# Kernel tuning notes

Measured on AMD Instinct MI355X. Metric: run time of the kernel, lower is better.

Reference implementation:

```python
import jax, jax.numpy as jnp
import numpy as np

N, E, D, H = 50000, 800000, 64, 4  # nodes, edges, dim_h, heads
NEG_SLOPE = 0.2
BN_EPS = 1e-5


def setup_inputs() -> dict:
    key = jax.random.key(0)
    ks = jax.random.split(key, 8)
    x = jax.random.normal(ks[0], (N, D), dtype=jnp.float32)
    edge_index = jax.random.randint(ks[1], (2, E), 0, N, dtype=jnp.int32)
    s = 1.0 / np.sqrt(D)
    W_lin = jax.random.normal(ks[2], (D, D), dtype=jnp.float32) * s
    b_lin = jnp.zeros((D,), dtype=jnp.float32)
    prelu_w = jnp.full((D,), 0.25, dtype=jnp.float32)
    W_gat = jax.random.normal(ks[3], (H * D, D), dtype=jnp.float32) * s  # maps D -> H*D
    att_src = jax.random.normal(ks[4], (H, D), dtype=jnp.float32) * 0.1
    att_dst = jax.random.normal(ks[5], (H, D), dtype=jnp.float32) * 0.1
    gat_bias = jnp.zeros((D,), dtype=jnp.float32)
    bn_gamma = jnp.ones((D,), dtype=jnp.float32)
    bn_beta = jnp.zeros((D,), dtype=jnp.float32)
    return dict(x=x, edge_index=edge_index, W_lin=W_lin, b_lin=b_lin,
                prelu_w=prelu_w, W_gat=W_gat, att_src=att_src, att_dst=att_dst,
                gat_bias=gat_bias, bn_gamma=bn_gamma, bn_beta=bn_beta)


def _gat_mod_fwd(x, edge_index, W_lin, b_lin, prelu_w, W_gat, att_src, att_dst,
                 gat_bias, bn_gamma, bn_beta):
    # --- pre linear + PReLU ---
    x = x @ W_lin.T + b_lin
    x = jnp.where(x >= 0, x, prelu_w * x)  # per-channel PReLU

    # --- GATConv (concat=False -> head mean), add_self_loops=True ---
    h = (x @ W_gat.T).reshape(N, H, D)              # [N,H,D]
    a_src = jnp.einsum('nhd,hd->nh', h, att_src)    # [N,H]
    a_dst = jnp.einsum('nhd,hd->nh', h, att_dst)    # [N,H]

    loop = jnp.arange(N, dtype=edge_index.dtype)
    src = jnp.concatenate([edge_index[0], loop])    # [E+N]
    dst = jnp.concatenate([edge_index[1], loop])

    e = jax.nn.leaky_relu(a_src[src] + a_dst[dst], NEG_SLOPE)   # [E+N, H]
    # segment softmax over destination nodes (self loops guarantee non-empty)
    emax = jax.ops.segment_max(e, dst, num_segments=N)          # [N,H]
    p = jnp.exp(e - emax[dst])
    denom = jax.ops.segment_sum(p, dst, num_segments=N)         # [N,H]
    alpha = p / denom[dst]                                      # [E+N,H]

    msg = h[src] * alpha[:, :, None]                            # [E+N,H,D]
    out = jax.ops.segment_sum(msg, dst, num_segments=N)         # [N,H,D]
    out = out.mean(axis=1) + gat_bias                           # [N,D]

    # --- BatchNorm1d (training: batch stats) + ReLU ---
    mean = out.mean(axis=0)
    var = out.var(axis=0)
    out = bn_gamma * (out - mean) * jax.lax.rsqrt(var + BN_EPS) + bn_beta
    return jax.nn.relu(out)


def reference(x, edge_index, W_lin, b_lin, prelu_w, W_gat, att_src, att_dst,
              gat_bias, bn_gamma, bn_beta):
    return _gat_mod_fwd(x, edge_index, W_lin, b_lin, prelu_w, W_gat, att_src,
                        att_dst, gat_bias, bn_gamma, bn_beta)
```

## Files before the change

kernel.cpp:

```cpp
#include <hip/hip_runtime.h>
#include <hip/hip_fp16.h>

#define NEG_SLOPE 0.2f
#define BN_EPS 1e-5f

constexpr int D = 64;
constexpr int H = 4;

constexpr int PSORT = 128;
constexpr int CHUNK_SHIFT = 13;
constexpr int CHUNK = 1 << CHUNK_SHIFT;
constexpr int MAXW2 = 12544;

typedef _Float16 half2_t __attribute__((ext_vector_type(2)));
typedef _Float16 half4_t __attribute__((ext_vector_type(4)));
typedef _Float16 half8_t __attribute__((ext_vector_type(8)));
typedef float f32x4_t __attribute__((ext_vector_type(4)));
typedef int i32x4 __attribute__((ext_vector_type(4)));

union Rec {
    i32x4 i4;
    struct { int idx; int pad; half4_t w; } f;
};

#define MFMA16(a, b, c) __builtin_amdgcn_mfma_f32_16x16x32_f16(a, b, c, 0, 0, 0)

#if __has_builtin(__builtin_amdgcn_fdot2)
#define FDOT2(a, b, c) __builtin_amdgcn_fdot2((a), (b), (c), false)
#else
#define FDOT2(a, b, c) ((c) + (float)(a)[0] * (float)(b)[0] + (float)(a)[1] * (float)(b)[1])
#endif

__device__ inline half2_t h2cast(unsigned int u) { return __builtin_bit_cast(half2_t, u); }

__device__ inline float lrelu(float v) { return (v >= 0.f) ? v : NEG_SLOPE * v; }

__device__ inline void split8(const float* p, bool ok, half8_t& hi, half8_t& lo) {
    float f[8];
    if (ok) {
        float4 a = *(const float4*)p;
        float4 b = *(const float4*)(p + 4);
        f[0] = a.x; f[1] = a.y; f[2] = a.z; f[3] = a.w;
        f[4] = b.x; f[5] = b.y; f[6] = b.z; f[7] = b.w;
    } else {
        #pragma unroll
        for (int j = 0; j < 8; j++) f[j] = 0.f;
    }
    #pragma unroll
    for (int j = 0; j < 8; j++) {
        _Float16 h = (_Float16)f[j];
        hi[j] = h;
        lo[j] = (_Float16)(f[j] - (float)h);
    }
}

__global__ __launch_bounds__(256) void k_node(
    const float* __restrict__ x,
    const float* __restrict__ W_lin, const float* __restrict__ b_lin,
    const float* __restrict__ prelu_w, const float* __restrict__ W_gat,
    const float* __restrict__ att_src, const float* __restrict__ att_dst,
    _Float16* __restrict__ hh, float* __restrict__ asrc_ws,
    float* __restrict__ adst_ws, int N)
{
    __shared__ _Float16 smem[32 * 264];
    _Float16* __restrict__ h_lds = smem;
    _Float16* __restrict__ x1hi  = smem;
    _Float16* __restrict__ x1lo  = smem + 32 * 72;

    const int t = threadIdx.x;
    const int w = t >> 6;
    const int l = t & 63;
    const int li = l & 15;
    const int lq = l >> 4;
    const int base = blockIdx.x * 32;
    const int nvalid = min(32, N - base);

    f32x4_t accA[2] = {};
    {
        half8_t blh[2], bll[2];
        const int n = 16 * w + li;
        #pragma unroll
        for (int ks = 0; ks < 2; ks++)
            split8(W_lin + n * 64 + 32 * ks + 8 * lq, true, blh[ks], bll[ks]);
        #pragma unroll
        for (int mt = 0; mt < 2; mt++) {
            const int row = base + 16 * mt + li;
            const bool ok = row < N;
            #pragma unroll
            for (int ks = 0; ks < 2; ks++) {
                half8_t ah, al;
                split8(x + (size_t)row * 64 + 32 * ks + 8 * lq, ok, ah, al);
                accA[mt] = MFMA16(ah, blh[ks], accA[mt]);
                accA[mt] = MFMA16(al, blh[ks], accA[mt]);
                accA[mt] = MFMA16(ah, bll[ks], accA[mt]);
            }
        }
    }

    {
        const int n = 16 * w + li;
        const float bl = b_lin[n];
        const float pw = prelu_w[n];
        #pragma unroll
        for (int mt = 0; mt < 2; mt++) {
            #pragma unroll
            for (int r = 0; r < 4; r++) {
                const int m = 16 * mt + lq * 4 + r;
                float v = accA[mt][r] + bl;
                v = (v >= 0.f) ? v : pw * v;
                _Float16 hi = (_Float16)v;
                x1hi[m * 72 + n] = hi;
                x1lo[m * 72 + n] = (_Float16)(v - (float)hi);
            }
        }
    }
    __syncthreads();

    half8_t xah[2][2], xal[2][2];
    #pragma unroll
    for (int mt = 0; mt < 2; mt++) {
        #pragma unroll
        for (int ks = 0; ks < 2; ks++) {
            const int off = (16 * mt + li) * 72 + 32 * ks + 8 * lq;
            xah[mt][ks] = *(const half8_t*)(&x1hi[off]);
            xal[mt][ks] = *(const half8_t*)(&x1lo[off]);
        }
    }
    f32x4_t accB[2][4] = {};
    #pragma unroll
    for (int nt = 0; nt < 4; nt++) {
        half8_t wh[2], wl[2];
        const int c = 64 * w + 16 * nt + li;
        #pragma unroll
        for (int ks = 0; ks < 2; ks++)
            split8(W_gat + (size_t)c * 64 + 32 * ks + 8 * lq, true, wh[ks], wl[ks]);
        #pragma unroll
        for (int mt = 0; mt < 2; mt++) {
            #pragma unroll
            for (int ks = 0; ks < 2; ks++) {
                accB[mt][nt] = MFMA16(xah[mt][ks], wh[ks], accB[mt][nt]);
                accB[mt][nt] = MFMA16(xal[mt][ks], wh[ks], accB[mt][nt]);
                accB[mt][nt] = MFMA16(xah[mt][ks], wl[ks], accB[mt][nt]);
            }
        }
    }

    {
        float asv[4], adv[4];
        #pragma unroll
        for (int nt = 0; nt < 4; nt++) {
            const int c = 64 * w + 16 * nt + li;
            asv[nt] = att_src[c];
            adv[nt] = att_dst[c];
        }
        #pragma unroll
        for (int mt = 0; mt < 2; mt++) {
            #pragma unroll
            for (int r = 0; r < 4; r++) {
                float s = 0.f, dsum = 0.f;
                #pragma unroll
                for (int nt = 0; nt < 4; nt++) {
                    s += accB[mt][nt][r] * asv[nt];
                    dsum += accB[mt][nt][r] * adv[nt];
                }
                #pragma unroll
                for (int off = 1; off < 16; off <<= 1) {
                    s += __shfl_xor(s, off, 64);
                    dsum += __shfl_xor(dsum, off, 64);
                }
                if (li == 0) {
                    const int m = 16 * mt + lq * 4 + r;
                    if (m < nvalid) {
                        asrc_ws[(size_t)(base + m) * H + w] = s;
                        adst_ws[(size_t)(base + m) * H + w] = dsum;
                    }
                }
            }
        }
    }

    __syncthreads();

    #pragma unroll
    for (int mt = 0; mt < 2; mt++) {
        #pragma unroll
        for (int nt = 0; nt < 4; nt++) {
            #pragma unroll
            for (int r = 0; r < 4; r++) {
                const int m = 16 * mt + lq * 4 + r;
                const int d = 16 * nt + li;
                h_lds[m * 264 + d * 4 + w] = (_Float16)accB[mt][nt][r];
            }
        }
    }
    __syncthreads();
    {
        const int chunks = nvalid * 32;
        const uint4* src = (const uint4*)h_lds;
        uint4* dst = (uint4*)(hh + (size_t)base * 256);
        for (int i = t; i < chunks; i += 256) {
            int row = i >> 5;
            int col = i & 31;
            dst[i] = src[row * 33 + col];
        }
    }
}

__global__ __launch_bounds__(1024) void k_hist(const int* __restrict__ ei,
                                               unsigned int* __restrict__ gcnt,
                                               int* __restrict__ rank,
                                               int E, int N2, int WTOT) {
    __shared__ unsigned int cnt[MAXW2];
    const int p = blockIdx.x & (PSORT - 1);
    const int pass = blockIdx.x >> 7;
    const int t = threadIdx.x;
    const int W2 = N2 >> 1;
    for (int i = t; i < W2; i += 1024) cnt[i] = 0;
    __syncthreads();
    const int e0 = p << CHUNK_SHIFT;
    const int e1 = min(E, e0 + CHUNK);
    const int nlo = pass * N2;
    for (int e = e0 + t; e < e1; e += 1024) {
        int dl = ei[E + e] - nlo;
        if ((unsigned)dl < (unsigned)N2) {
            const unsigned int sh = (unsigned)(dl & 1) * 16;
            unsigned int old = atomicAdd(&cnt[dl >> 1], 1u << sh);
            rank[e] = (int)((old >> sh) & 0xffffu);
        }
    }
    __syncthreads();
    unsigned int* dst = gcnt + (size_t)p * WTOT + (size_t)pass * W2;
    for (int i = t; i < W2; i += 1024) dst[i] = cnt[i];
}

__global__ __launch_bounds__(256) void k_off(unsigned int* __restrict__ gcnt,
                                             int* __restrict__ gcount,
                                             int* __restrict__ offs,
                                             int* __restrict__ deg,
                                             int N, int WTOT) {
    __shared__ int sm[256];
    __shared__ int sbase;
    const int t = threadIdx.x;
    const int i = blockIdx.x * 256 + t;
    int d0 = 0, d1 = 0;
    if (i < WTOT) {
        unsigned int run = 0;
        for (int pb = 0; pb < PSORT; pb += 32) {
            unsigned int c[32];
            #pragma unroll
            for (int j = 0; j < 32; j++)
                c[j] = gcnt[(size_t)(pb + j) * WTOT + i];
            #pragma unroll
            for (int j = 0; j < 32; j++) {
                unsigned int cc = c[j];
                gcnt[(size_t)(pb + j) * WTOT + i] = run;
                run += cc;
            }
        }
        d0 = (int)(run & 0xffffu);
        d1 = (int)(run >> 16);
    }
    int v = d0 + d1;
    sm[t] = v;
    __syncthreads();
    for (int off = 1; off < 256; off <<= 1) {
        int u = (t >= off) ? sm[t - off] : 0;
        __syncthreads();
        sm[t] += u;
        __syncthreads();
    }
    if (t == 255) sbase = atomicAdd(gcount, sm[255]);
    __syncthreads();
    const int base = sbase + sm[t] - v;
    const int n0 = 2 * i;
    if (n0 < N)     { offs[n0] = base;          deg[n0] = d0; }
    if (n0 + 1 < N) { offs[n0 + 1] = base + d0; deg[n0 + 1] = d1; }
}

__global__ __launch_bounds__(256) void k_fill(const int* __restrict__ ei,
                                              const unsigned int* __restrict__ gcnt,
                                              const int* __restrict__ offs,
                                              const int* __restrict__ rank,
                                              const float* __restrict__ asrc,
                                              const float* __restrict__ adst,
                                              i32x4* __restrict__ recs,
                                              int E, int WTOT) {
    int e = blockIdx.x * 256 + threadIdx.x;
    if (e >= E) return;
    int s = ei[e];
    int d = ei[E + e];
    int p = e >> CHUNK_SHIFT;
    const unsigned int sh = (unsigned)(d & 1) * 16;
    int pr = (int)((gcnt[(size_t)p * WTOT + (d >> 1)] >> sh) & 0xffffu);
    int pos = offs[d] + pr + rank[e];
    float4 a = *(const float4*)(asrc + (size_t)s * H);
    float4 b = *(const float4*)(adst + (size_t)d * H);
    Rec r;
    r.f.idx = s;
    r.f.pad = 0;
    r.f.w[0] = (_Float16)__expf(lrelu(a.x + b.x));
    r.f.w[1] = (_Float16)__expf(lrelu(a.y + b.y));
    r.f.w[2] = (_Float16)__expf(lrelu(a.z + b.z));
    r.f.w[3] = (_Float16)__expf(lrelu(a.w + b.w));
    recs[pos] = r.i4;
}

__device__ inline void edge_pair(const i32x4 ra, const i32x4 rb,
                                 const uint2 ha, const uint2 hb,
                                 float& den0, float& den1, float& den2, float& den3,
                                 float& acc0, float& acc1, float& acc2, float& acc3)
{
    const half2_t one2 = h2cast(0x3C003C00u);
    unsigned int wp0 = __builtin_amdgcn_perm((unsigned int)rb.z, (unsigned int)ra.z, 0x05040100u);
    unsigned int wp1 = __builtin_amdgcn_perm((unsigned int)rb.z, (unsigned int)ra.z, 0x07060302u);
    unsigned int wp2 = __builtin_amdgcn_perm((unsigned int)rb.w, (unsigned int)ra.w, 0x05040100u);
    unsigned int wp3 = __builtin_amdgcn_perm((unsigned int)rb.w, (unsigned int)ra.w, 0x07060302u);
    unsigned int hp0 = __builtin_amdgcn_perm(hb.x, ha.x, 0x05040100u);
    unsigned int hp1 = __builtin_amdgcn_perm(hb.x, ha.x, 0x07060302u);
    unsigned int hp2 = __builtin_amdgcn_perm(hb.y, ha.y, 0x05040100u);
    unsigned int hp3 = __builtin_amdgcn_perm(hb.y, ha.y, 0x07060302u);
    den0 = FDOT2(h2cast(wp0), one2, den0);
    den1 = FDOT2(h2cast(wp1), one2, den1);
    den2 = FDOT2(h2cast(wp2), one2, den2);
    den3 = FDOT2(h2cast(wp3), one2, den3);
    acc0 = FDOT2(h2cast(wp0), h2cast(hp0), acc0);
    acc1 = FDOT2(h2cast(wp1), h2cast(hp1), acc1);
    acc2 = FDOT2(h2cast(wp2), h2cast(hp2), acc2);
    acc3 = FDOT2(h2cast(wp3), h2cast(hp3), acc3);
}

__global__ __launch_bounds__(256) void k_agg(
    const float* __restrict__ asrc, const float* __restrict__ adst,
    const int* __restrict__ offs, const int* __restrict__ deg,
    const i32x4* __restrict__ recs, const uint2* __restrict__ hh2,
    float* __restrict__ out, int N)
{
    int wid = (blockIdx.x * 256 + threadIdx.x) >> 6;
    int lane = threadIdx.x & 63;
    if (wid >= N) return;
    const int i = wid;

    float4 b = *(const float4*)(adst + (size_t)i * H);
    float4 a0 = *(const float4*)(asrc + (size_t)i * H);
    float ws0 = __expf(lrelu(a0.x + b.x));
    float ws1 = __expf(lrelu(a0.y + b.y));
    float ws2 = __expf(lrelu(a0.z + b.z));
    float ws3 = __expf(lrelu(a0.w + b.w));

    const int beg = __builtin_amdgcn_readfirstlane(offs[i]);
    const int dg  = __builtin_amdgcn_readfirstlane(deg[i]);

    float den0 = ws0, den1 = ws1, den2 = ws2, den3 = ws3;
    float acc0, acc1, acc2, acc3;
    {
        uint2 hv = hh2[(size_t)i * D + lane];
        half2_t s01 = h2cast(hv.x), s23 = h2cast(hv.y);
        acc0 = ws0 * (float)s01[0];
        acc1 = ws1 * (float)s01[1];
        acc2 = ws2 * (float)s23[0];
        acc3 = ws3 * (float)s23[1];
    }

    const int nfull = dg & ~7;
    int k = 0;
    for (; k < nfull; k += 8) {
        i32x4 rr[8];
        #pragma unroll
        for (int j = 0; j < 8; j++)
            rr[j] = __builtin_nontemporal_load(recs + beg + k + j);
        uint2 hv[8];
        #pragma unroll
        for (int j = 0; j < 8; j++)
            hv[j] = hh2[(size_t)rr[j].x * D + lane];
        #pragma unroll
        for (int j = 0; j < 8; j += 2)
            edge_pair(rr[j], rr[j + 1], hv[j], hv[j + 1],
                      den0, den1, den2, den3, acc0, acc1, acc2, acc3);
    }
    if (k < dg) {
        i32x4 rr[8];
        #pragma unroll
        for (int j = 0; j < 8; j++) {
            int kk = min(k + j, dg - 1);
            i32x4 r = __builtin_nontemporal_load(recs + beg + kk);
            if (k + j >= dg) { r.z = 0; r.w = 0; }
            rr[j] = r;
        }
        uint2 hv[8];
        #pragma unroll
        for (int j = 0; j < 8; j++)
            hv[j] = hh2[(size_t)rr[j].x * D + lane];
        #pragma unroll
        for (int j = 0; j < 8; j += 2)
            edge_pair(rr[j], rr[j + 1], hv[j], hv[j + 1],
                      den0, den1, den2, den3, acc0, acc1, acc2, acc3);
    }

    out[(size_t)i * D + lane] =
        0.25f * (acc0 / den0 + acc1 / den1 + acc2 / den2 + acc3 / den3);
}

__global__ __launch_bounds__(256) void k_bn_stats(const float* __restrict__ out,
                                                  float* __restrict__ sums,
                                                  int total) {
    const int t = threadIdx.x;
    const int stride = gridDim.x * 256;
    float s = 0.f, sq = 0.f;
    for (int idx = blockIdx.x * 256 + t; idx < total; idx += stride) {
        float v = out[idx];
        s += v;
        sq += v * v;
    }
    __shared__ float ls[256], lq[256];
    ls[t] = s;
    lq[t] = sq;
    __syncthreads();
    if (t < 64) {
        s = ls[t] + ls[t + 64] + ls[t + 128] + ls[t + 192];
        sq = lq[t] + lq[t + 64] + lq[t + 128] + lq[t + 192];
        atomicAdd(&sums[t], s);
        atomicAdd(&sums[64 + t], sq);
    }
}

__global__ __launch_bounds__(256) void k_bn_apply(float* __restrict__ out,
                                                  const float* __restrict__ sums,
                                                  const float* __restrict__ gamma,
                                                  const float* __restrict__ beta,
                                                  int total, float invN) {
    int idx = blockIdx.x * 256 + threadIdx.x;
    if (idx >= total) return;
    int c = idx & 63;
    float mean = sums[c] * invN;
    float var = sums[64 + c] * invN - mean * mean;
    float y = gamma[c] * (out[idx] - mean) * rsqrtf(var + BN_EPS) + beta[c];
    out[idx] = fmaxf(y, 0.f);
}

extern "C" void kernel_launch(void* const* d_in, const int* in_sizes, int n_in,
                              void* d_out, int out_size, void* d_ws, size_t ws_size,
                              hipStream_t stream) {
    const float* x       = (const float*)d_in[0];
    const int*   ei      = (const int*)d_in[1];
    const float* W_lin   = (const float*)d_in[2];
    const float* b_lin   = (const float*)d_in[3];
    const float* prelu_w = (const float*)d_in[4];
    const float* W_gat   = (const float*)d_in[5];
    const float* att_src = (const float*)d_in[6];
    const float* att_dst = (const float*)d_in[7];
    const float* bn_gamma = (const float*)d_in[9];
    const float* bn_beta  = (const float*)d_in[10];
    float* out = (float*)d_out;

    const int N = in_sizes[0] / D;
    const int E = in_sizes[1] / 2;

    int N2 = (N + 1) / 2;
    N2 = (N2 + 1) & ~1;
    const int WTOT = N2;

    char* wp = (char*)d_ws;
    _Float16* hh = (_Float16*)wp;      wp += (size_t)N * D * H * sizeof(_Float16);
    float* asrc  = (float*)wp;          wp += (size_t)N * H * sizeof(float);
    float* adst  = (float*)wp;          wp += (size_t)N * H * sizeof(float);
    char* zero_base = wp;
    float* sums  = (float*)wp;          wp += 2 * D * sizeof(float);
    int* gcount  = (int*)wp;            wp += 4 * sizeof(int);
    size_t zero_bytes = (size_t)(wp - zero_base);
    int* offs    = (int*)wp;            wp += (size_t)((N + 3) & ~3) * sizeof(int);
    int* deg     = (int*)wp;            wp += (size_t)((N + 3) & ~3) * sizeof(int);
    int* rank    = (int*)wp;            wp += (size_t)((E + 3) & ~3) * sizeof(int);
    i32x4* recs  = (i32x4*)wp;          wp += (size_t)E * sizeof(i32x4);
    unsigned int* gcnt;
    if ((size_t)PSORT * WTOT * sizeof(unsigned int) <= (size_t)out_size) {
        gcnt = (unsigned int*)d_out;
    } else {
        gcnt = (unsigned int*)wp;
        wp += (size_t)PSORT * WTOT * sizeof(unsigned int);
    }
    (void)ws_size; (void)n_in;

    const int total = N * D;
    const int NB1 = (N + 31) / 32;
    const int NBS = 2 * PSORT;
    const int NBO = (WTOT + 255) / 256;

    hipMemsetAsync(zero_base, 0, zero_bytes, stream);
    hipLaunchKernelGGL(k_node, dim3(NB1), dim3(256), 0, stream,
                       x, W_lin, b_lin, prelu_w, W_gat, att_src, att_dst,
                       hh, asrc, adst, N);
    hipLaunchKernelGGL(k_hist, dim3(NBS), dim3(1024), 0, stream,
                       ei, gcnt, rank, E, N2, WTOT);
    hipLaunchKernelGGL(k_off, dim3(NBO), dim3(256), 0, stream,
                       gcnt, gcount, offs, deg, N, WTOT);
    hipLaunchKernelGGL(k_fill, dim3((E + 255) / 256), dim3(256), 0, stream,
                       ei, gcnt, offs, rank, asrc, adst, recs, E, WTOT);
    hipLaunchKernelGGL(k_agg, dim3((N + 3) / 4), dim3(256), 0, stream,
                       asrc, adst, offs, deg, recs, (const uint2*)hh, out, N);
    hipLaunchKernelGGL(k_bn_stats, dim3(1024), dim3(256), 0, stream,
                       out, sums, total);
    hipLaunchKernelGGL(k_bn_apply, dim3((total + 255) / 256), dim3(256), 0, stream,
                       out, sums, bn_gamma, bn_beta, total, 1.f / (float)N);
}
```

Baseline: 246.3 us.

## Fuse node transform with histogram, fold BN stats into aggregation, drop memset

Merges the node-feature kernel and the destination histogram into one launch, with extra blocks doing histogram work on 8 smaller node groups that use 256-thread blocks and fit in the node kernel's shared memory. The aggregation kernel now walks 8 nodes per wave and accumulates BatchNorm sum and sum-of-squares itself, atomically adding into 32 sliced buffers that the apply kernel reduces. The memset is removed: zeroing of sums moves into k_off and gcount is reset by the histogram blocks. This removes two launches plus the memset and a full reread of the output, at the cost of more histogram passes over the edge list and per-element slice reductions in the apply kernel.

```diff
diff --git a/kernel.cpp b/kernel.cpp
--- a/kernel.cpp
+++ b/kernel.cpp
@@ -10,7 +10,8 @@
 constexpr int PSORT = 128;
 constexpr int CHUNK_SHIFT = 13;
 constexpr int CHUNK = 1 << CHUNK_SHIFT;
-constexpr int MAXW2 = 12544;
+constexpr int NGROUPS = 8;
+constexpr int BN_SLICES = 32;
 
 typedef _Float16 half2_t __attribute__((ext_vector_type(2)));
 typedef _Float16 half4_t __attribute__((ext_vector_type(4)));
@@ -54,20 +55,50 @@
     }
 }
 
-__global__ __launch_bounds__(256) void k_node(
+__global__ __launch_bounds__(256) void k_nodehist(
     const float* __restrict__ x,
     const float* __restrict__ W_lin, const float* __restrict__ b_lin,
     const float* __restrict__ prelu_w, const float* __restrict__ W_gat,
     const float* __restrict__ att_src, const float* __restrict__ att_dst,
     _Float16* __restrict__ hh, float* __restrict__ asrc_ws,
-    float* __restrict__ adst_ws, int N)
+    float* __restrict__ adst_ws, const int* __restrict__ ei,
+    unsigned int* __restrict__ gcnt, int* __restrict__ rank,
+    int* __restrict__ gcount, int N, int E, int NB1, int NG, int WTOT)
 {
-    __shared__ _Float16 smem[32 * 264];
+    __shared__ unsigned int smem4[4224];
+    const int t = threadIdx.x;
+
+    if ((int)blockIdx.x >= NB1) {
+        unsigned int* cnt = smem4;
+        const int hb = blockIdx.x - NB1;
+        const int p = hb & (PSORT - 1);
+        const int g = hb >> 7;
+        const int Wg = NG >> 1;
+        for (int i = t; i < Wg; i += 256) cnt[i] = 0;
+        __syncthreads();
+        const int e0 = p << CHUNK_SHIFT;
+        const int e1 = min(E, e0 + CHUNK);
+        const int nlo = g * NG;
+        for (int e = e0 + t; e < e1; e += 256) {
+            int dl = ei[E + e] - nlo;
+            if ((unsigned)dl < (unsigned)NG) {
+                const unsigned int sh = (unsigned)(dl & 1) * 16;
+                unsigned int old = atomicAdd(&cnt[dl >> 1], 1u << sh);
+                rank[e] = (int)((old >> sh) & 0xffffu);
+            }
+        }
+        __syncthreads();
+        unsigned int* dst = gcnt + (size_t)p * WTOT + (size_t)g * Wg;
+        for (int i = t; i < Wg; i += 256) dst[i] = cnt[i];
+        if (hb == 0 && t == 0) gcount[0] = 0;
+        return;
+    }
+
+    _Float16* smem = (_Float16*)smem4;
     _Float16* __restrict__ h_lds = smem;
     _Float16* __restrict__ x1hi  = smem;
     _Float16* __restrict__ x1lo  = smem + 32 * 72;
 
-    const int t = threadIdx.x;
     const int w = t >> 6;
     const int l = t & 63;
     const int li = l & 15;
@@ -206,38 +237,15 @@
     }
 }
 
-__global__ __launch_bounds__(1024) void k_hist(const int* __restrict__ ei,
-                                               unsigned int* __restrict__ gcnt,
-                                               int* __restrict__ rank,
-                                               int E, int N2, int WTOT) {
-    __shared__ unsigned int cnt[MAXW2];
-    const int p = blockIdx.x & (PSORT - 1);
-    const int pass = blockIdx.x >> 7;
-    const int t = threadIdx.x;
-    const int W2 = N2 >> 1;
-    for (int i = t; i < W2; i += 1024) cnt[i] = 0;
-    __syncthreads();
-    const int e0 = p << CHUNK_SHIFT;
-    const int e1 = min(E, e0 + CHUNK);
-    const int nlo = pass * N2;
-    for (int e = e0 + t; e < e1; e += 1024) {
-        int dl = ei[E + e] - nlo;
-        if ((unsigned)dl < (unsigned)N2) {
-            const unsigned int sh = (unsigned)(dl & 1) * 16;
-            unsigned int old = atomicAdd(&cnt[dl >> 1], 1u << sh);
-            rank[e] = (int)((old >> sh) & 0xffffu);
-        }
-    }
-    __syncthreads();
-    unsigned int* dst = gcnt + (size_t)p * WTOT + (size_t)pass * W2;
-    for (int i = t; i < W2; i += 1024) dst[i] = cnt[i];
-}
-
 __global__ __launch_bounds__(256) void k_off(unsigned int* __restrict__ gcnt,
                                              int* __restrict__ gcount,
                                              int* __restrict__ offs,
                                              int* __restrict__ deg,
+                                             float* __restrict__ sums,
                                              int N, int WTOT) {
+    if (blockIdx.x == 0) {
+        for (int j = threadIdx.x; j < BN_SLICES * 128; j += 256) sums[j] = 0.f;
+    }
     __shared__ int sm[256];
     __shared__ int sbase;
     const int t = threadIdx.x;
@@ -333,93 +341,91 @@
     const float* __restrict__ asrc, const float* __restrict__ adst,
     const int* __restrict__ offs, const int* __restrict__ deg,
     const i32x4* __restrict__ recs, const uint2* __restrict__ hh2,
-    float* __restrict__ out, int N)
+    float* __restrict__ out, float* __restrict__ sums, int N)
 {
-    int wid = (blockIdx.x * 256 + threadIdx.x) >> 6;
-    int lane = threadIdx.x & 63;
-    if (wid >= N) return;
-    const int i = wid;
-
-    float4 b = *(const float4*)(adst + (size_t)i * H);
-    float4 a0 = *(const float4*)(asrc + (size_t)i * H);
-    float ws0 = __expf(lrelu(a0.x + b.x));
-    float ws1 = __expf(lrelu(a0.y + b.y));
-    float ws2 = __expf(lrelu(a0.z + b.z));
-    float ws3 = __expf(lrelu(a0.w + b.w));
-
-    const int beg = __builtin_amdgcn_readfirstlane(offs[i]);
-    const int dg  = __builtin_amdgcn_readfirstlane(deg[i]);
-
-    float den0 = ws0, den1 = ws1, den2 = ws2, den3 = ws3;
-    float acc0, acc1, acc2, acc3;
-    {
-        uint2 hv = hh2[(size_t)i * D + lane];
-        half2_t s01 = h2cast(hv.x), s23 = h2cast(hv.y);
-        acc0 = ws0 * (float)s01[0];
-        acc1 = ws1 * (float)s01[1];
-        acc2 = ws2 * (float)s23[0];
-        acc3 = ws3 * (float)s23[1];
-    }
-
-    const int nfull = dg & ~7;
-    int k = 0;
-    for (; k < nfull; k += 8) {
-        i32x4 rr[8];
-        #pragma unroll
-        for (int j = 0; j < 8; j++)
-            rr[j] = __builtin_nontemporal_load(recs + beg + k + j);
-        uint2 hv[8];
-        #pragma unroll
-        for (int j = 0; j < 8; j++)
-            hv[j] = hh2[(size_t)rr[j].x * D + lane];
-        #pragma unroll
-        for (int j = 0; j < 8; j += 2)
-            edge_pair(rr[j], rr[j + 1], hv[j], hv[j + 1],
-                      den0, den1, den2, den3, acc0, acc1, acc2, acc3);
-    }
-    if (k < dg) {
-        i32x4 rr[8];
-        #pragma unroll
-        for (int j = 0; j < 8; j++) {
-            int kk = min(k + j, dg - 1);
-            i32x4 r = __builtin_nontemporal_load(recs + beg + kk);
-            if (k + j >= dg) { r.z = 0; r.w = 0; }
-            rr[j] = r;
-        }
-        uint2 hv[8];
-        #pragma unroll
-        for (int j = 0; j < 8; j++)
-            hv[j] = hh2[(size_t)rr[j].x * D + lane];
-        #pragma unroll
-        for (int j = 0; j < 8; j += 2)
-            edge_pair(rr[j], rr[j + 1], hv[j], hv[j + 1],
-                      den0, den1, den2, den3, acc0, acc1, acc2, acc3);
-    }
-
-    out[(size_t)i * D + lane] =
-        0.25f * (acc0 / den0 + acc1 / den1 + acc2 / den2 + acc3 / den3);
-}
-
-__global__ __launch_bounds__(256) void k_bn_stats(const float* __restrict__ out,
-                                                  float* __restrict__ sums,
-                                                  int total) {
     const int t = threadIdx.x;
-    const int stride = gridDim.x * 256;
-    float s = 0.f, sq = 0.f;
-    for (int idx = blockIdx.x * 256 + t; idx < total; idx += stride) {
-        float v = out[idx];
-        s += v;
-        sq += v * v;
-    }
+    const int w = t >> 6;
+    const int lane = t & 63;
+    const int gw = blockIdx.x * 4 + w;
+    const int n0 = gw * 8;
+
+    float sAcc = 0.f, qAcc = 0.f;
+    for (int ni = 0; ni < 8; ni++) {
+        const int i = n0 + ni;
+        if (i >= N) break;
+
+        float4 b = *(const float4*)(adst + (size_t)i * H);
+        float4 a0 = *(const float4*)(asrc + (size_t)i * H);
+        float ws0 = __expf(lrelu(a0.x + b.x));
+        float ws1 = __expf(lrelu(a0.y + b.y));
+        float ws2 = __expf(lrelu(a0.z + b.z));
+        float ws3 = __expf(lrelu(a0.w + b.w));
+
+        const int beg = __builtin_amdgcn_readfirstlane(offs[i]);
+        const int dg  = __builtin_amdgcn_readfirstlane(deg[i]);
+
+        float den0 = ws0, den1 = ws1, den2 = ws2, den3 = ws3;
+        float acc0, acc1, acc2, acc3;
+        {
+            uint2 hv = hh2[(size_t)i * D + lane];
+            half2_t s01 = h2cast(hv.x), s23 = h2cast(hv.y);
+            acc0 = ws0 * (float)s01[0];
+            acc1 = ws1 * (float)s01[1];
+            acc2 = ws2 * (float)s23[0];
+            acc3 = ws3 * (float)s23[1];
+        }
+
+        const int nfull = dg & ~7;
+        int k = 0;
+        for (; k < nfull; k += 8) {
+            i32x4 rr[8];
+            #pragma unroll
+            for (int j = 0; j < 8; j++)
+                rr[j] = __builtin_nontemporal_load(recs + beg + k + j);
+            uint2 hv[8];
+            #pragma unroll
+            for (int j = 0; j < 8; j++)
+                hv[j] = hh2[(size_t)rr[j].x * D + lane];
+            #pragma unroll
+            for (int j = 0; j < 8; j += 2)
+                edge_pair(rr[j], rr[j + 1], hv[j], hv[j + 1],
+                          den0, den1, den2, den3, acc0, acc1, acc2, acc3);
+        }
+        if (k < dg) {
+            i32x4 rr[8];
+            #pragma unroll
+            for (int j = 0; j < 8; j++) {
+                int kk = min(k + j, dg - 1);
+                i32x4 r = __builtin_nontemporal_load(recs + beg + kk);
+                if (k + j >= dg) { r.z = 0; r.w = 0; }
+                rr[j] = r;
+            }
+            uint2 hv[8];
+            #pragma unroll
+            for (int j = 0; j < 8; j++)
+                hv[j] = hh2[(size_t)rr[j].x * D + lane];
+            #pragma unroll
+            for (int j = 0; j < 8; j += 2)
+                edge_pair(rr[j], rr[j + 1], hv[j], hv[j + 1],
+                          den0, den1, den2, den3, acc0, acc1, acc2, acc3);
+        }
+
+        float v = 0.25f * (acc0 / den0 + acc1 / den1 + acc2 / den2 + acc3 / den3);
+        out[(size_t)i * D + lane] = v;
+        sAcc += v;
+        qAcc += v * v;
+    }
+
     __shared__ float ls[256], lq[256];
-    ls[t] = s;
-    lq[t] = sq;
+    ls[t] = sAcc;
+    lq[t] = qAcc;
     __syncthreads();
     if (t < 64) {
-        s = ls[t] + ls[t + 64] + ls[t + 128] + ls[t + 192];
-        sq = lq[t] + lq[t + 64] + lq[t + 128] + lq[t + 192];
-        atomicAdd(&sums[t], s);
-        atomicAdd(&sums[64 + t], sq);
+        float s = ls[t] + ls[t + 64] + ls[t + 128] + ls[t + 192];
+        float q = lq[t] + lq[t + 64] + lq[t + 128] + lq[t + 192];
+        const int sl = blockIdx.x & (BN_SLICES - 1);
+        atomicAdd(&sums[sl * 128 + t], s);
+        atomicAdd(&sums[sl * 128 + 64 + t], q);
     }
 }
 
@@ -431,8 +437,14 @@
     int idx = blockIdx.x * 256 + threadIdx.x;
     if (idx >= total) return;
     int c = idx & 63;
-    float mean = sums[c] * invN;
-    float var = sums[64 + c] * invN - mean * mean;
+    float s = 0.f, q = 0.f;
+    #pragma unroll
+    for (int p = 0; p < BN_SLICES; p++) {
+        s += sums[p * 128 + c];
+        q += sums[p * 128 + 64 + c];
+    }
+    float mean = s * invN;
+    float var = q * invN - mean * mean;
     float y = gamma[c] * (out[idx] - mean) * rsqrtf(var + BN_EPS) + beta[c];
     out[idx] = fmaxf(y, 0.f);
 }
@@ -455,18 +467,15 @@
     const int N = in_sizes[0] / D;
     const int E = in_sizes[1] / 2;
 
-    int N2 = (N + 1) / 2;
-    N2 = (N2 + 1) & ~1;
-    const int WTOT = N2;
+    const int NG = 2 * ((N + 15) / 16);
+    const int WTOT = NGROUPS * (NG >> 1);
 
     char* wp = (char*)d_ws;
     _Float16* hh = (_Float16*)wp;      wp += (size_t)N * D * H * sizeof(_Float16);
     float* asrc  = (float*)wp;          wp += (size_t)N * H * sizeof(float);
     float* adst  = (float*)wp;          wp += (size_t)N * H * sizeof(float);
-    char* zero_base = wp;
-    float* sums  = (float*)wp;          wp += 2 * D * sizeof(float);
+    float* sums  = (float*)wp;          wp += (size_t)BN_SLICES * 128 * sizeof(float);
     int* gcount  = (int*)wp;            wp += 4 * sizeof(int);
-    size_t zero_bytes = (size_t)(wp - zero_base);
     int* offs    = (int*)wp;            wp += (size_t)((N + 3) & ~3) * sizeof(int);
     int* deg     = (int*)wp;            wp += (size_t)((N + 3) & ~3) * sizeof(int);
     int* rank    = (int*)wp;            wp += (size_t)((E + 3) & ~3) * sizeof(int);
@@ -482,23 +491,19 @@
 
     const int total = N * D;
     const int NB1 = (N + 31) / 32;
-    const int NBS = 2 * PSORT;
+    const int NBU = NB1 + NGROUPS * PSORT;
     const int NBO = (WTOT + 255) / 256;
-
-    hipMemsetAsync(zero_base, 0, zero_bytes, stream);
-    hipLaunchKernelGGL(k_node, dim3(NB1), dim3(256), 0, stream,
+    const int NBA = (N + 31) / 32;
+
+    hipLaunchKernelGGL(k_nodehist, dim3(NBU), dim3(256), 0, stream,
                        x, W_lin, b_lin, prelu_w, W_gat, att_src, att_dst,
-                       hh, asrc, adst, N);
-    hipLaunchKernelGGL(k_hist, dim3(NBS), dim3(1024), 0, stream,
-                       ei, gcnt, rank, E, N2, WTOT);
+                       hh, asrc, adst, ei, gcnt, rank, gcount, N, E, NB1, NG, WTOT);
     hipLaunchKernelGGL(k_off, dim3(NBO), dim3(256), 0, stream,
-                       gcnt, gcount, offs, deg, N, WTOT);
+                       gcnt, gcount, offs, deg, sums, N, WTOT);
     hipLaunchKernelGGL(k_fill, dim3((E + 255) / 256), dim3(256), 0, stream,
                        ei, gcnt, offs, rank, asrc, adst, recs, E, WTOT);
-    hipLaunchKernelGGL(k_agg, dim3((N + 3) / 4), dim3(256), 0, stream,
-                       asrc, adst, offs, deg, recs, (const uint2*)hh, out, N);
-    hipLaunchKernelGGL(k_bn_stats, dim3(1024), dim3(256), 0, stream,
-                       out, sums, total);
+    hipLaunchKernelGGL(k_agg, dim3(NBA), dim3(256), 0, stream,
+                       asrc, adst, offs, deg, recs, (const uint2*)hh, out, sums, N);
     hipLaunchKernelGGL(k_bn_apply, dim3((total + 255) / 256), dim3(256), 0, stream,
                        out, sums, bn_gamma, bn_beta, total, 1.f / (float)N);
 }
```

New measurement: 245.2 us. Within noise of the previous version (-0.4%).
